# Kernel optimization log

Measured on AMD Instinct MI355X. Metric: run time of the kernel, lower is better.

## Reference

```python
import jax, jax.numpy as jnp
import numpy as np

N_NODES = 2048
IN_FEAT = 512
N_HIDDEN = 512   # layer1 out_features (concat over 8 heads -> 64 per head)
N_CLASSES = 256  # output layer out_features (1 head, averaged)
N_HEADS = 8
NEG_SLOPE = 0.2


def _gat_layer(h, adj, W, a, n_heads, n_hid, is_concat):
    """GraphAttentionLayer (v1) forward, dropout=0 (eval).
    e[i,j,h] = leakyrelu(attn([g_i ; g_j])) decomposes as
    leakyrelu(a_l.g_i + a_r.g_j) since attn is linear."""
    n = h.shape[0]
    g = (h @ W).reshape(n, n_heads, n_hid)           # [n, H, F']
    a_l, a_r = a[:n_hid], a[n_hid:]                  # attn weight split
    s_l = jnp.einsum('ihf,f->ih', g, a_l)            # [n, H]
    s_r = jnp.einsum('jhf,f->jh', g, a_r)            # [n, H]
    e = jax.nn.leaky_relu(s_l[:, None, :] + s_r[None, :, :], NEG_SLOPE)  # [n,n,H]
    e = jnp.where(adj == 0, -jnp.inf, e)             # adj [n,n,1] broadcasts over heads
    attn = jax.nn.softmax(e, axis=1)                 # softmax over neighbors j
    out = jnp.einsum('ijh,jhf->ihf', attn, g)        # [n, H, F']
    if is_concat:
        return out.reshape(n, n_heads * n_hid)
    return out.mean(axis=1)


def setup_inputs() -> dict:
    key = jax.random.key(0)
    ks = jax.random.split(key, 6)
    x = jax.random.normal(ks[0], (N_NODES, IN_FEAT), dtype=jnp.float32)
    adj = jax.random.randint(ks[1], (N_NODES, N_NODES, 1), 0, 2, dtype=jnp.int32)
    # self loops so every row of the softmax has at least one valid entry
    diag = jnp.arange(N_NODES)
    adj = adj.at[diag, diag, 0].set(1)
    W1 = jax.random.normal(ks[2], (IN_FEAT, N_HIDDEN), dtype=jnp.float32) / np.sqrt(IN_FEAT)
    a1 = jax.random.normal(ks[3], (2 * (N_HIDDEN // N_HEADS),), dtype=jnp.float32) / np.sqrt(2 * (N_HIDDEN // N_HEADS))
    W2 = jax.random.normal(ks[4], (N_HIDDEN, N_CLASSES), dtype=jnp.float32) / np.sqrt(N_HIDDEN)
    a2 = jax.random.normal(ks[5], (2 * N_CLASSES,), dtype=jnp.float32) / np.sqrt(2 * N_CLASSES)
    return {"x": x, "adj_mat": adj, "W1": W1, "a1": a1, "W2": W2, "a2": a2}


def reference(x, adj_mat, W1, a1, W2, a2):
    # GAT.forward with dropout=0 (eval mode)
    h = _gat_layer(x, adj_mat, W1, a1, N_HEADS, N_HIDDEN // N_HEADS, True)
    h = jax.nn.elu(h)
    out = _gat_layer(h, adj_mat, W2, a2, 1, N_CLASSES, False)
    return out
```

## Files before the change

### kernel.cpp

```cpp
#include <hip/hip_runtime.h>
#include <hip/hip_bf16.h>
#include <math.h>

#define NN 2048
#define LOG2E 1.4426950408889634f

typedef __attribute__((ext_vector_type(8))) short short8;
typedef __attribute__((ext_vector_type(4))) short s16x4;
typedef __attribute__((ext_vector_type(4))) float f32x4;

__device__ inline unsigned short f2bfu(float f) {
    __hip_bfloat16 h = __float2bfloat16(f);
    return *reinterpret_cast<const unsigned short*>(&h);
}
__device__ inline short f2bfs(float f) {
    __hip_bfloat16 h = __float2bfloat16(f);
    return *reinterpret_cast<const short*>(&h);
}
__device__ inline float bfu2f(unsigned short u) {
    return __uint_as_float(((unsigned int)u) << 16);
}

__global__ __launch_bounds__(256) void pack_adj(
    const int* __restrict__ adj, unsigned long long* __restrict__ adjm,
    float* __restrict__ zeros)
{
    const int t = threadIdx.x, w = t >> 6, l = t & 63;
    if (blockIdx.x < 144) zeros[blockIdx.x * 256 + t] = 0.f;
    const int gw = blockIdx.x * 4 + w;
    const int row = gw >> 5, ch = gw & 31;
    const int v = adj[(size_t)row * NN + ch * 64 + l];
    const unsigned long long bm = __ballot(v != 0);
    if (l == 0) adjm[gw] = bm;
}

__global__ __launch_bounds__(256) void pack_ws(
    const float* __restrict__ W1, unsigned short* __restrict__ w1H, unsigned short* __restrict__ w1L,
    const float* __restrict__ W2, unsigned short* __restrict__ w2H, unsigned short* __restrict__ w2L)
{
    const int t = threadIdx.x, w = t >> 6, l = t & 63;
    const int gq = l >> 4, n16 = l & 15;
    int f = blockIdx.x * 4 + w;
    const float* B; unsigned short *bH, *bL; int N;
    if (f < 512) { B = W1; bH = w1H; bL = w1L; N = 512; }
    else         { B = W2; bH = w2H; bL = w2L; N = 256; f -= 512; }
    const int KT = 16;
    const int nt = f / KT, kt = f - nt * KT;
    const int col = nt * 16 + n16;
    unsigned short uh[8], ul[8];
    #pragma unroll
    for (int e = 0; e < 8; ++e) {
        const int k = kt * 32 + 4 * gq + (e & 3) + 16 * (e >> 2);
        const float v = B[(size_t)k * N + col];
        const unsigned short h = f2bfu(v);
        uh[e] = h;
        ul[e] = f2bfu(v - bfu2f(h));
    }
    *(short8*)&bH[(size_t)f * 512 + l * 8] = *(const short8*)uh;
    *(short8*)&bL[(size_t)f * 512 + l * 8] = *(const short8*)ul;
}

__global__ __launch_bounds__(256) void pack_a_split(
    const float* __restrict__ A, unsigned short* __restrict__ aH,
    unsigned short* __restrict__ aL, int K)
{
    const int t = threadIdx.x, w = t >> 6, l = t & 63;
    const int gq = l >> 4, n16 = l & 15;
    const int KT = K >> 5;
    const int f = blockIdx.x * 4 + w;
    const int mt = f / KT, kt = f - mt * KT;
    const int row = mt * 16 + n16;
    const int k0 = kt * 32 + 4 * gq;
    unsigned short uh[8], ul[8];
    #pragma unroll
    for (int eh = 0; eh < 2; ++eh) {
        const float4 v4 = *(const float4*)&A[(size_t)row * K + k0 + 16 * eh];
        const float vv[4] = {v4.x, v4.y, v4.z, v4.w};
        #pragma unroll
        for (int c = 0; c < 4; ++c) {
            const float v = vv[c];
            const unsigned short h = f2bfu(v);
            uh[4 * eh + c] = h;
            ul[4 * eh + c] = f2bfu(v - bfu2f(h));
        }
    }
    *(short8*)&aH[(size_t)f * 512 + l * 8] = *(const short8*)uh;
    *(short8*)&aL[(size_t)f * 512 + l * 8] = *(const short8*)ul;
}

__global__ __launch_bounds__(256, 2) void gemm_fused(
    const unsigned short* __restrict__ aH, const unsigned short* __restrict__ aL,
    const unsigned short* __restrict__ bH, const unsigned short* __restrict__ bL,
    const float* __restrict__ av, unsigned short* __restrict__ gpO,
    float* __restrict__ slO, float* __restrict__ srO,
    int KT, int dh, int NT)
{
    const int t = threadIdx.x, w = t >> 6, l = t & 63;
    const int gq = l >> 4, n16 = l & 15;
    const int mt = blockIdx.x * 4 + w;
    const int cb = blockIdx.y;
    const int nt0 = cb * 4;
    const size_t abase = (size_t)mt * KT * 512 + l * 8;

    f32x4 acc[4];
    #pragma unroll
    for (int nt = 0; nt < 4; ++nt) acc[nt] = f32x4{0.f, 0.f, 0.f, 0.f};

#define GL(aH_v, aL_v, bH_v, bL_v, kt_) do {                                     \
    const int kk_ = (kt_);                                                       \
    aH_v = *(const short8*)&aH[abase + (size_t)kk_ * 512];                       \
    aL_v = *(const short8*)&aL[abase + (size_t)kk_ * 512];                       \
    _Pragma("unroll")                                                            \
    for (int nt_ = 0; nt_ < 4; ++nt_) {                                          \
        const size_t bo_ = ((size_t)(nt0 + nt_) * KT + kk_) * 512 + l * 8;       \
        bH_v[nt_] = *(const short8*)&bH[bo_];                                    \
        bL_v[nt_] = *(const short8*)&bL[bo_];                                    \
    }                                                                            \
} while (0)

#define GC(aH_v, aL_v, bH_v, bL_v) do {                                          \
    _Pragma("unroll")                                                            \
    for (int nt_ = 0; nt_ < 4; ++nt_) {                                          \
        acc[nt_] = __builtin_amdgcn_mfma_f32_16x16x32_bf16(aH_v, bH_v[nt_], acc[nt_], 0, 0, 0); \
        acc[nt_] = __builtin_amdgcn_mfma_f32_16x16x32_bf16(aH_v, bL_v[nt_], acc[nt_], 0, 0, 0); \
        acc[nt_] = __builtin_amdgcn_mfma_f32_16x16x32_bf16(aL_v, bH_v[nt_], acc[nt_], 0, 0, 0); \
    }                                                                            \
} while (0)

    short8 aHa, aLa, bHa[4], bLa[4], aHb, aLb, bHb[4], bLb[4];
    GL(aHa, aLa, bHa, bLa, 0);
    GL(aHb, aLb, bHb, bLb, 1);
    for (int kt = 0; kt < KT; kt += 2) {
        GC(aHa, aLa, bHa, bLa);
        if (kt + 2 < KT) GL(aHa, aLa, bHa, bLa, kt + 2);
        GC(aHb, aLb, bHb, bLb);
        if (kt + 3 < KT) GL(aHb, aLb, bHb, bLb, kt + 3);
    }
#undef GL
#undef GC

    #pragma unroll
    for (int nt = 0; nt < 4; ++nt) {
        s16x4 u;
        #pragma unroll
        for (int c = 0; c < 4; ++c) u[c] = (short)f2bfu(acc[nt][c]);
        const int f = (mt >> 1) * NT + (nt0 + nt);
        *(s16x4*)&gpO[(size_t)f * 512 + l * 8 + 4 * (mt & 1)] = u;
    }
    const float* al = av;
    const float* ar = av + dh;
    float pl[4] = {0.f, 0.f, 0.f, 0.f}, pr[4] = {0.f, 0.f, 0.f, 0.f};
    #pragma unroll
    for (int nt = 0; nt < 4; ++nt) {
        const int q = (cb * 64 + 16 * nt + n16) & (dh - 1);
        const float wl = al[q], wr_ = ar[q];
        #pragma unroll
        for (int r = 0; r < 4; ++r) { pl[r] += acc[nt][r] * wl; pr[r] += acc[nt][r] * wr_; }
    }
    #pragma unroll
    for (int r = 0; r < 4; ++r) {
        #pragma unroll
        for (int off = 1; off < 16; off <<= 1) {
            pl[r] += __shfl_xor(pl[r], off);
            pr[r] += __shfl_xor(pr[r], off);
        }
    }
    if (n16 == 0) {
        const int hbase = (dh == 64 ? cb : 0) * NN;
        #pragma unroll
        for (int r = 0; r < 4; ++r) {
            const int grow = 16 * mt + 4 * gq + r;
            atomicAdd(&slO[hbase + grow], pl[r] * LOG2E);
            atomicAdd(&srO[hbase + grow], pr[r] * LOG2E);
        }
    }
}

template<int BM, int OUTMODE>
__global__ __launch_bounds__(512, 4) void attn_mfma5(
    const float* __restrict__ slv, const float* __restrict__ srv,
    const unsigned short* __restrict__ gp, const unsigned long long* __restrict__ adjm,
    float* __restrict__ out, unsigned short* __restrict__ aoH, unsigned short* __restrict__ aoL,
    int out_cols, int hsel, int do_elu, int ntg_total)
{
    constexpr int WR = BM / 16;
    constexpr int NJS = 8 / WR;
    constexpr int NITER = (NN / 64) / NJS;
    const int t = threadIdx.x, w = t >> 6, l = t & 63;
    const int gq = l >> 4, n16 = l & 15;
    const int wr = w % WR, js = w / WR;
    const int i0 = blockIdx.x * BM;
    const int cb = blockIdx.y;
    const int h = (hsel < 0) ? cb : hsel;
    const int ntg0 = cb * 4;
    const int arow = i0 + 16 * wr + n16;
    const float* srh = srv + (size_t)h * NN;
    const float sl_reg = slv[(size_t)h * NN + arow];

    __shared__ float accs[8][4][4][65];
    __shared__ float zp[NJS][BM];

    f32x4 acc[4];
    #pragma unroll
    for (int nt = 0; nt < 4; ++nt) acc[nt] = f32x4{0.f, 0.f, 0.f, 0.f};
    float zacc = 0.f;

#define LOADT(am_, bf_, tile_) do {                                              \
    const int tl_ = (tile_);                                                     \
    am_ = adjm[(size_t)arow * 32 + tl_];                                         \
    _Pragma("unroll")                                                            \
    for (int s_ = 0; s_ < 2; ++s_)                                               \
        _Pragma("unroll")                                                        \
        for (int nt_ = 0; nt_ < 4; ++nt_)                                        \
            bf_[s_][nt_] = *(const short8*)&gp[                                  \
                (size_t)((2 * tl_ + s_) * ntg_total + ntg0 + nt_) * 512 + l * 8];\
} while (0)

#define COMPT(am_, bf_, tile_) do {                                              \
    const int tl_ = (tile_);                                                     \
    f32x4 sr4_[4];                                                               \
    _Pragma("unroll")                                                            \
    for (int q_ = 0; q_ < 4; ++q_)                                               \
        sr4_[q_] = *(const f32x4*)&srh[64 * tl_ + 32 * (q_ >> 1) + 16 * (q_ & 1) + 4 * gq]; \
    short8 af_[2];                                                               \
    _Pragma("unroll")                                                            \
    for (int s_ = 0; s_ < 2; ++s_) {                                             \
        const unsigned am32_ = (unsigned)(am_ >> (32 * s_ + 4 * gq));            \
        _Pragma("unroll")                                                        \
        for (int hb_ = 0; hb_ < 2; ++hb_) {                                      \
            const f32x4 s4_ = sr4_[2 * s_ + hb_];                                \
            _Pragma("unroll")                                                    \
            for (int c_ = 0; c_ < 4; ++c_) {                                     \
                float f_ = sl_reg + s4_[c_];                                     \
                f_ = fmaxf(f_, 0.2f * f_);                                       \
                float wv_ = __builtin_amdgcn_exp2f(f_);                          \
                const int msk_ = (int)(am32_ << (31 - (c_ + 16 * hb_))) >> 31;   \
                wv_ = __int_as_float(__float_as_int(wv_) & msk_);                \
                zacc += wv_;                                                     \
                af_[s_][4 * hb_ + c_] = f2bfs(wv_);                              \
            }                                                                    \
        }                                                                        \
    }                                                                            \
    _Pragma("unroll")                                                            \
    for (int s_ = 0; s_ < 2; ++s_)                                               \
        _Pragma("unroll")                                                        \
        for (int nt_ = 0; nt_ < 4; ++nt_)                                        \
            acc[nt_] = __builtin_amdgcn_mfma_f32_16x16x32_bf16(                  \
                af_[s_], bf_[s_][nt_], acc[nt_], 0, 0, 0);                       \
} while (0)

    unsigned long long amA, amB;
    short8 bfA[2][4], bfB[2][4];

    LOADT(amA, bfA, js);
    LOADT(amB, bfB, js + NJS);

    for (int k = 0; k < NITER; k += 2) {
        COMPT(amA, bfA, js + k * NJS);
        {
            const int kn = (k + 2 < NITER) ? (k + 2) : (NITER - 1);
            LOADT(amA, bfA, js + kn * NJS);
        }
        COMPT(amB, bfB, js + (k + 1) * NJS);
        {
            const int kn = (k + 3 < NITER) ? (k + 3) : (NITER - 1);
            LOADT(amB, bfB, js + kn * NJS);
        }
    }
#undef LOADT
#undef COMPT

    zacc += __shfl_xor(zacc, 16);
    zacc += __shfl_xor(zacc, 32);
    if (l < 16) zp[js][16 * wr + l] = zacc;
    #pragma unroll
    for (int nt = 0; nt < 4; ++nt)
        #pragma unroll
        for (int r = 0; r < 4; ++r)
            accs[w][nt][r][l] = acc[nt][r];
    __syncthreads();

    if constexpr (OUTMODE == 0) {
        #pragma unroll
        for (int idx = 0; idx < WR * 2; ++idx) {
            const int flat = w + 8 * idx;
            const int wr2 = flat >> 4, rem = flat & 15, nt = rem >> 2, r = rem & 3;
            const int ro = 16 * wr2 + 4 * gq + r;
            float z = 0.f, v = 0.f;
            #pragma unroll
            for (int jj = 0; jj < NJS; ++jj) {
                z += zp[jj][ro];
                v += accs[jj * WR + wr2][nt][r][l];
            }
            float o = v / z;
            if (do_elu) o = (o > 0.f) ? o : (__builtin_amdgcn_exp2f(o * LOG2E) - 1.f);
            out[(size_t)(i0 + ro) * out_cols + cb * 64 + nt * 16 + n16] = o;
        }
    } else {
        const int mtl = (w >> 1) & 1, ktl = w & 1, eh = w >> 2;
        const int rowl = l & 15, colq = l >> 4;
        const int grow = 16 * mtl + rowl;
        float z = 0.f;
        #pragma unroll
        for (int jj = 0; jj < NJS; ++jj) z += zp[jj][grow];
        const float rz = 1.0f / z;
        const int wr2 = mtl, srcr = rowl & 3, srcgq = (rowl >> 2) & 3;
        unsigned short uh[4], ul[4];
        #pragma unroll
        for (int c = 0; c < 4; ++c) {
            const int col = 32 * ktl + 16 * eh + 4 * colq + c;
            const int nt = col >> 4, c16 = col & 15;
            float v = 0.f;
            #pragma unroll
            for (int jj = 0; jj < NJS; ++jj)
                v += accs[jj * WR + wr2][nt][srcr][srcgq * 16 + c16];
            float o = v * rz;
            o = (o > 0.f) ? o : (__builtin_amdgcn_exp2f(o * LOG2E) - 1.f);
            const unsigned short hi = f2bfu(o);
            uh[c] = hi;
            ul[c] = f2bfu(o - bfu2f(hi));
        }
        const int mt = (i0 >> 4) + mtl, kt = 2 * cb + ktl;
        const size_t off = ((size_t)mt * 16 + kt) * 512 + l * 8 + 4 * eh;
        *(s16x4*)&aoH[off] = *(const s16x4*)uh;
        *(s16x4*)&aoL[off] = *(const s16x4*)ul;
    }
}

extern "C" void kernel_launch(void* const* d_in, const int* in_sizes, int n_in,
                              void* d_out, int out_size, void* d_ws, size_t ws_size,
                              hipStream_t stream)
{
    const float* x   = (const float*)d_in[0];
    const int*   adj = (const int*)  d_in[1];
    const float* W1  = (const float*)d_in[2];
    const float* a1  = (const float*)d_in[3];
    const float* W2  = (const float*)d_in[4];
    const float* a2  = (const float*)d_in[5];
    float* out = (float*)d_out;

    float* sl1 = (float*)d_ws;
    float* sr1 = sl1 + 8 * 2048;
    float* sl2 = sr1 + 8 * 2048;
    float* sr2 = sl2 + 2048;
    unsigned long long* adjm = (unsigned long long*)(sr2 + 2048);
    unsigned short* gp1 = (unsigned short*)(adjm + 65536);
    unsigned short* gp2 = gp1 + 2048 * 512;
    unsigned short* axH = gp2 + 1024 * 512;
    unsigned short* axL = axH + 2048 * 512;
    unsigned short* ahH = axL + 2048 * 512;
    unsigned short* ahL = ahH + 2048 * 512;
    unsigned short* w1H = ahL + 2048 * 512;
    unsigned short* w1L = w1H + 512 * 512;
    unsigned short* w2H = w1L + 512 * 512;
    unsigned short* w2L = w2H + 256 * 512;

    pack_adj<<<dim3(16384), 256, 0, stream>>>(adj, adjm, sl1);
    pack_ws<<<dim3(192), 256, 0, stream>>>(W1, w1H, w1L, W2, w2H, w2L);
    pack_a_split<<<dim3(512), 256, 0, stream>>>(x, axH, axL, 512);

    gemm_fused<<<dim3(32, 8), 256, 0, stream>>>(axH, axL, w1H, w1L, a1, gp1, sl1, sr1, 16, 64, 32);
    attn_mfma5<32, 1><<<dim3(64, 8), 512, 0, stream>>>(sl1, sr1, gp1, adjm,
                                                       nullptr, ahH, ahL, 512, -1, 1, 32);

    gemm_fused<<<dim3(32, 4), 256, 0, stream>>>(ahH, ahL, w2H, w2L, a2, gp2, sl2, sr2, 16, 256, 16);
    attn_mfma5<16, 0><<<dim3(128, 4), 512, 0, stream>>>(sl2, sr2, gp2, adjm,
                                                        out, nullptr, nullptr, 256, 0, 0, 16);
}
```

Measured before the change: 63.85 us.

## Merge prep kernels and restructure attention to share B fragments across row tiles

Folds the three packing kernels into a single prep launch, removing two kernel launches. The attention kernel now has each wave process all row tiles (MT) against one j-subtile, so each loaded gp fragment feeds MT MFMAs instead of splitting rows across waves. Adjacency is read as 32-bit half-words per subtile, and the layer-1 epilogue is staged in two halves to fit shared memory. The trade-off is more registers per wave and extra barriers in the epilogue.

```diff
diff --git a/kernel.cpp b/kernel.cpp
--- a/kernel.cpp
+++ b/kernel.cpp
@@ -21,71 +21,63 @@
     return __uint_as_float(((unsigned int)u) << 16);
 }
 
-__global__ __launch_bounds__(256) void pack_adj(
+__global__ __launch_bounds__(256) void prep(
     const int* __restrict__ adj, unsigned long long* __restrict__ adjm,
-    float* __restrict__ zeros)
+    float* __restrict__ zeros,
+    const float* __restrict__ W1, unsigned short* __restrict__ w1H, unsigned short* __restrict__ w1L,
+    const float* __restrict__ W2, unsigned short* __restrict__ w2H, unsigned short* __restrict__ w2L,
+    const float* __restrict__ x, unsigned short* __restrict__ axH, unsigned short* __restrict__ axL)
 {
-    const int t = threadIdx.x, w = t >> 6, l = t & 63;
-    if (blockIdx.x < 144) zeros[blockIdx.x * 256 + t] = 0.f;
-    const int gw = blockIdx.x * 4 + w;
-    const int row = gw >> 5, ch = gw & 31;
-    const int v = adj[(size_t)row * NN + ch * 64 + l];
-    const unsigned long long bm = __ballot(v != 0);
-    if (l == 0) adjm[gw] = bm;
-}
-
-__global__ __launch_bounds__(256) void pack_ws(
-    const float* __restrict__ W1, unsigned short* __restrict__ w1H, unsigned short* __restrict__ w1L,
-    const float* __restrict__ W2, unsigned short* __restrict__ w2H, unsigned short* __restrict__ w2L)
-{
-    const int t = threadIdx.x, w = t >> 6, l = t & 63;
+    const int b = blockIdx.x, t = threadIdx.x, w = t >> 6, l = t & 63;
     const int gq = l >> 4, n16 = l & 15;
-    int f = blockIdx.x * 4 + w;
-    const float* B; unsigned short *bH, *bL; int N;
-    if (f < 512) { B = W1; bH = w1H; bL = w1L; N = 512; }
-    else         { B = W2; bH = w2H; bL = w2L; N = 256; f -= 512; }
-    const int KT = 16;
-    const int nt = f / KT, kt = f - nt * KT;
-    const int col = nt * 16 + n16;
-    unsigned short uh[8], ul[8];
-    #pragma unroll
-    for (int e = 0; e < 8; ++e) {
-        const int k = kt * 32 + 4 * gq + (e & 3) + 16 * (e >> 2);
-        const float v = B[(size_t)k * N + col];
-        const unsigned short h = f2bfu(v);
-        uh[e] = h;
-        ul[e] = f2bfu(v - bfu2f(h));
-    }
-    *(short8*)&bH[(size_t)f * 512 + l * 8] = *(const short8*)uh;
-    *(short8*)&bL[(size_t)f * 512 + l * 8] = *(const short8*)ul;
-}
-
-__global__ __launch_bounds__(256) void pack_a_split(
-    const float* __restrict__ A, unsigned short* __restrict__ aH,
-    unsigned short* __restrict__ aL, int K)
-{
-    const int t = threadIdx.x, w = t >> 6, l = t & 63;
-    const int gq = l >> 4, n16 = l & 15;
-    const int KT = K >> 5;
-    const int f = blockIdx.x * 4 + w;
-    const int mt = f / KT, kt = f - mt * KT;
-    const int row = mt * 16 + n16;
-    const int k0 = kt * 32 + 4 * gq;
-    unsigned short uh[8], ul[8];
-    #pragma unroll
-    for (int eh = 0; eh < 2; ++eh) {
-        const float4 v4 = *(const float4*)&A[(size_t)row * K + k0 + 16 * eh];
-        const float vv[4] = {v4.x, v4.y, v4.z, v4.w};
-        #pragma unroll
-        for (int c = 0; c < 4; ++c) {
-            const float v = vv[c];
-            const unsigned short h = f2bfu(v);
-            uh[4 * eh + c] = h;
-            ul[4 * eh + c] = f2bfu(v - bfu2f(h));
-        }
-    }
-    *(short8*)&aH[(size_t)f * 512 + l * 8] = *(const short8*)uh;
-    *(short8*)&aL[(size_t)f * 512 + l * 8] = *(const short8*)ul;
+    {
+        const int gw = b * 4 + w;
+        const int row = gw >> 5, ch = gw & 31;
+        const int v = adj[(size_t)row * NN + ch * 64 + l];
+        const unsigned long long bm = __ballot(v != 0);
+        if (l == 0) adjm[gw] = bm;
+    }
+    if (b < 144) {
+        zeros[b * 256 + t] = 0.f;
+    } else if (b >= 256 && b < 448) {
+        int f = (b - 256) * 4 + w;
+        const float* B; unsigned short *bH, *bL; int N;
+        if (f < 512) { B = W1; bH = w1H; bL = w1L; N = 512; }
+        else         { B = W2; bH = w2H; bL = w2L; N = 256; f -= 512; }
+        const int nt = f >> 4, kt = f & 15;
+        const int col = nt * 16 + n16;
+        unsigned short uh[8], ul[8];
+        #pragma unroll
+        for (int e = 0; e < 8; ++e) {
+            const int k = kt * 32 + 4 * gq + (e & 3) + 16 * (e >> 2);
+            const float v = B[(size_t)k * N + col];
+            const unsigned short hi = f2bfu(v);
+            uh[e] = hi;
+            ul[e] = f2bfu(v - bfu2f(hi));
+        }
+        *(short8*)&bH[(size_t)f * 512 + l * 8] = *(const short8*)uh;
+        *(short8*)&bL[(size_t)f * 512 + l * 8] = *(const short8*)ul;
+    } else if (b >= 448 && b < 960) {
+        const int f = (b - 448) * 4 + w;
+        const int mt = f >> 4, kt = f & 15;
+        const int row = mt * 16 + n16;
+        const int k0 = kt * 32 + 4 * gq;
+        unsigned short uh[8], ul[8];
+        #pragma unroll
+        for (int eh = 0; eh < 2; ++eh) {
+            const float4 v4 = *(const float4*)&x[(size_t)row * 512 + k0 + 16 * eh];
+            const float vv[4] = {v4.x, v4.y, v4.z, v4.w};
+            #pragma unroll
+            for (int c = 0; c < 4; ++c) {
+                const float v = vv[c];
+                const unsigned short hi = f2bfu(v);
+                uh[4 * eh + c] = hi;
+                ul[4 * eh + c] = f2bfu(v - bfu2f(hi));
+            }
+        }
+        *(short8*)&axH[(size_t)f * 512 + l * 8] = *(const short8*)uh;
+        *(short8*)&axL[(size_t)f * 512 + l * 8] = *(const short8*)ul;
+    }
 }
 
 __global__ __launch_bounds__(256, 2) void gemm_fused(
@@ -176,154 +168,174 @@
     }
 }
 
-template<int BM, int OUTMODE>
-__global__ __launch_bounds__(512, 4) void attn_mfma5(
+template<int MT, int OUTMODE>
+__global__ __launch_bounds__(512, 4) void attn_mfma6(
     const float* __restrict__ slv, const float* __restrict__ srv,
-    const unsigned short* __restrict__ gp, const unsigned long long* __restrict__ adjm,
+    const unsigned short* __restrict__ gp, const unsigned int* __restrict__ adjm32,
     float* __restrict__ out, unsigned short* __restrict__ aoH, unsigned short* __restrict__ aoL,
     int out_cols, int hsel, int do_elu, int ntg_total)
 {
-    constexpr int WR = BM / 16;
-    constexpr int NJS = 8 / WR;
-    constexpr int NITER = (NN / 64) / NJS;
     const int t = threadIdx.x, w = t >> 6, l = t & 63;
     const int gq = l >> 4, n16 = l & 15;
-    const int wr = w % WR, js = w / WR;
-    const int i0 = blockIdx.x * BM;
+    const int i0 = blockIdx.x * (MT * 16);
     const int cb = blockIdx.y;
     const int h = (hsel < 0) ? cb : hsel;
     const int ntg0 = cb * 4;
-    const int arow = i0 + 16 * wr + n16;
     const float* srh = srv + (size_t)h * NN;
-    const float sl_reg = slv[(size_t)h * NN + arow];
-
-    __shared__ float accs[8][4][4][65];
-    __shared__ float zp[NJS][BM];
-
-    f32x4 acc[4];
-    #pragma unroll
-    for (int nt = 0; nt < 4; ++nt) acc[nt] = f32x4{0.f, 0.f, 0.f, 0.f};
-    float zacc = 0.f;
-
-#define LOADT(am_, bf_, tile_) do {                                              \
+    int arow[MT];
+    float slr[MT];
+    #pragma unroll
+    for (int mt = 0; mt < MT; ++mt) {
+        arow[mt] = i0 + 16 * mt + n16;
+        slr[mt] = slv[(size_t)h * NN + arow[mt]];
+    }
+
+    __shared__ float accs_raw[8320];
+    __shared__ float zp[8][MT * 16];
+
+    f32x4 acc[MT][4];
+    float zacc[MT];
+    #pragma unroll
+    for (int mt = 0; mt < MT; ++mt) {
+        zacc[mt] = 0.f;
+        #pragma unroll
+        for (int nt = 0; nt < 4; ++nt) acc[mt][nt] = f32x4{0.f, 0.f, 0.f, 0.f};
+    }
+
+#define LOADH(bf_, sr_, am_, tile_, s_) do {                                     \
     const int tl_ = (tile_);                                                     \
-    am_ = adjm[(size_t)arow * 32 + tl_];                                         \
-    _Pragma("unroll")                                                            \
-    for (int s_ = 0; s_ < 2; ++s_)                                               \
-        _Pragma("unroll")                                                        \
-        for (int nt_ = 0; nt_ < 4; ++nt_)                                        \
-            bf_[s_][nt_] = *(const short8*)&gp[                                  \
-                (size_t)((2 * tl_ + s_) * ntg_total + ntg0 + nt_) * 512 + l * 8];\
+    _Pragma("unroll")                                                            \
+    for (int nt_ = 0; nt_ < 4; ++nt_)                                            \
+        bf_[nt_] = *(const short8*)&gp[                                          \
+            (size_t)((2 * tl_ + (s_)) * ntg_total + ntg0 + nt_) * 512 + l * 8];  \
+    _Pragma("unroll")                                                            \
+    for (int hb_ = 0; hb_ < 2; ++hb_)                                            \
+        sr_[hb_] = *(const f32x4*)&srh[64 * tl_ + 32 * (s_) + 16 * hb_ + 4 * gq];\
+    _Pragma("unroll")                                                            \
+    for (int mt_ = 0; mt_ < MT; ++mt_)                                           \
+        am_[mt_] = adjm32[((size_t)arow[mt_] * 32 + tl_) * 2 + (s_)];            \
 } while (0)
 
-#define COMPT(am_, bf_, tile_) do {                                              \
-    const int tl_ = (tile_);                                                     \
-    f32x4 sr4_[4];                                                               \
-    _Pragma("unroll")                                                            \
-    for (int q_ = 0; q_ < 4; ++q_)                                               \
-        sr4_[q_] = *(const f32x4*)&srh[64 * tl_ + 32 * (q_ >> 1) + 16 * (q_ & 1) + 4 * gq]; \
-    short8 af_[2];                                                               \
-    _Pragma("unroll")                                                            \
-    for (int s_ = 0; s_ < 2; ++s_) {                                             \
-        const unsigned am32_ = (unsigned)(am_ >> (32 * s_ + 4 * gq));            \
+#define COMPH(bf_, sr_, am_) do {                                                \
+    short8 af_[MT];                                                              \
+    _Pragma("unroll")                                                            \
+    for (int mt_ = 0; mt_ < MT; ++mt_) {                                         \
+        const unsigned am32_ = am_[mt_] >> (4 * gq);                             \
         _Pragma("unroll")                                                        \
         for (int hb_ = 0; hb_ < 2; ++hb_) {                                      \
-            const f32x4 s4_ = sr4_[2 * s_ + hb_];                                \
+            const f32x4 s4_ = sr_[hb_];                                          \
             _Pragma("unroll")                                                    \
             for (int c_ = 0; c_ < 4; ++c_) {                                     \
-                float f_ = sl_reg + s4_[c_];                                     \
+                float f_ = slr[mt_] + s4_[c_];                                   \
                 f_ = fmaxf(f_, 0.2f * f_);                                       \
                 float wv_ = __builtin_amdgcn_exp2f(f_);                          \
                 const int msk_ = (int)(am32_ << (31 - (c_ + 16 * hb_))) >> 31;   \
                 wv_ = __int_as_float(__float_as_int(wv_) & msk_);                \
-                zacc += wv_;                                                     \
-                af_[s_][4 * hb_ + c_] = f2bfs(wv_);                              \
+                zacc[mt_] += wv_;                                                \
+                af_[mt_][4 * hb_ + c_] = f2bfs(wv_);                             \
             }                                                                    \
         }                                                                        \
     }                                                                            \
     _Pragma("unroll")                                                            \
-    for (int s_ = 0; s_ < 2; ++s_)                                               \
+    for (int mt_ = 0; mt_ < MT; ++mt_)                                           \
         _Pragma("unroll")                                                        \
         for (int nt_ = 0; nt_ < 4; ++nt_)                                        \
-            acc[nt_] = __builtin_amdgcn_mfma_f32_16x16x32_bf16(                  \
-                af_[s_], bf_[s_][nt_], acc[nt_], 0, 0, 0);                       \
+            acc[mt_][nt_] = __builtin_amdgcn_mfma_f32_16x16x32_bf16(             \
+                af_[mt_], bf_[nt_], acc[mt_][nt_], 0, 0, 0);                     \
 } while (0)
 
-    unsigned long long amA, amB;
-    short8 bfA[2][4], bfB[2][4];
-
-    LOADT(amA, bfA, js);
-    LOADT(amB, bfB, js + NJS);
-
-    for (int k = 0; k < NITER; k += 2) {
-        COMPT(amA, bfA, js + k * NJS);
-        {
-            const int kn = (k + 2 < NITER) ? (k + 2) : (NITER - 1);
-            LOADT(amA, bfA, js + kn * NJS);
-        }
-        COMPT(amB, bfB, js + (k + 1) * NJS);
-        {
-            const int kn = (k + 3 < NITER) ? (k + 3) : (NITER - 1);
-            LOADT(amB, bfB, js + kn * NJS);
-        }
-    }
-#undef LOADT
-#undef COMPT
-
-    zacc += __shfl_xor(zacc, 16);
-    zacc += __shfl_xor(zacc, 32);
-    if (l < 16) zp[js][16 * wr + l] = zacc;
-    #pragma unroll
-    for (int nt = 0; nt < 4; ++nt)
-        #pragma unroll
-        for (int r = 0; r < 4; ++r)
-            accs[w][nt][r][l] = acc[nt][r];
-    __syncthreads();
+    unsigned amA[MT], amB[MT];
+    f32x4 srA[2], srB[2];
+    short8 bfA[4], bfB[4];
+
+    LOADH(bfA, srA, amA, w, 0);
+    LOADH(bfB, srB, amB, w, 1);
+    #pragma unroll
+    for (int k = 0; k < 4; ++k) {
+        const int tn = (k < 3) ? (w + 8 * (k + 1)) : (w + 8 * k);
+        COMPH(bfA, srA, amA);
+        LOADH(bfA, srA, amA, tn, 0);
+        COMPH(bfB, srB, amB);
+        LOADH(bfB, srB, amB, tn, 1);
+    }
+#undef LOADH
+#undef COMPH
+
+    #pragma unroll
+    for (int mt = 0; mt < MT; ++mt) {
+        zacc[mt] += __shfl_xor(zacc[mt], 16);
+        zacc[mt] += __shfl_xor(zacc[mt], 32);
+    }
+    if (l < 16) {
+        #pragma unroll
+        for (int mt = 0; mt < MT; ++mt) zp[w][16 * mt + l] = zacc[mt];
+    }
 
     if constexpr (OUTMODE == 0) {
         #pragma unroll
-        for (int idx = 0; idx < WR * 2; ++idx) {
+        for (int nt = 0; nt < 4; ++nt)
+            #pragma unroll
+            for (int r = 0; r < 4; ++r)
+                accs_raw[((w * 4 + nt) * 4 + r) * 65 + l] = acc[0][nt][r];
+        __syncthreads();
+        #pragma unroll
+        for (int idx = 0; idx < 2; ++idx) {
             const int flat = w + 8 * idx;
-            const int wr2 = flat >> 4, rem = flat & 15, nt = rem >> 2, r = rem & 3;
-            const int ro = 16 * wr2 + 4 * gq + r;
+            const int nt = flat >> 2, r = flat & 3;
+            const int ro = 4 * gq + r;
             float z = 0.f, v = 0.f;
             #pragma unroll
-            for (int jj = 0; jj < NJS; ++jj) {
+            for (int jj = 0; jj < 8; ++jj) {
                 z += zp[jj][ro];
-                v += accs[jj * WR + wr2][nt][r][l];
+                v += accs_raw[((jj * 4 + nt) * 4 + r) * 65 + l];
             }
             float o = v / z;
             if (do_elu) o = (o > 0.f) ? o : (__builtin_amdgcn_exp2f(o * LOG2E) - 1.f);
             out[(size_t)(i0 + ro) * out_cols + cb * 64 + nt * 16 + n16] = o;
         }
     } else {
-        const int mtl = (w >> 1) & 1, ktl = w & 1, eh = w >> 2;
+        const int mtl = w & 1, eh = (w >> 1) & 1;
         const int rowl = l & 15, colq = l >> 4;
-        const int grow = 16 * mtl + rowl;
-        float z = 0.f;
-        #pragma unroll
-        for (int jj = 0; jj < NJS; ++jj) z += zp[jj][grow];
-        const float rz = 1.0f / z;
-        const int wr2 = mtl, srcr = rowl & 3, srcgq = (rowl >> 2) & 3;
-        unsigned short uh[4], ul[4];
-        #pragma unroll
-        for (int c = 0; c < 4; ++c) {
-            const int col = 32 * ktl + 16 * eh + 4 * colq + c;
-            const int nt = col >> 4, c16 = col & 15;
-            float v = 0.f;
+        #pragma unroll
+        for (int h2 = 0; h2 < 2; ++h2) {
             #pragma unroll
-            for (int jj = 0; jj < NJS; ++jj)
-                v += accs[jj * WR + wr2][nt][srcr][srcgq * 16 + c16];
-            float o = v * rz;
-            o = (o > 0.f) ? o : (__builtin_amdgcn_exp2f(o * LOG2E) - 1.f);
-            const unsigned short hi = f2bfu(o);
-            uh[c] = hi;
-            ul[c] = f2bfu(o - bfu2f(hi));
-        }
-        const int mt = (i0 >> 4) + mtl, kt = 2 * cb + ktl;
-        const size_t off = ((size_t)mt * 16 + kt) * 512 + l * 8 + 4 * eh;
-        *(s16x4*)&aoH[off] = *(const s16x4*)uh;
-        *(s16x4*)&aoL[off] = *(const s16x4*)ul;
+            for (int mt = 0; mt < MT; ++mt)
+                #pragma unroll
+                for (int ntl = 0; ntl < 2; ++ntl)
+                    #pragma unroll
+                    for (int r = 0; r < 4; ++r)
+                        accs_raw[(((w * 2 + mt) * 2 + ntl) * 4 + r) * 65 + l] =
+                            acc[mt][2 * h2 + ntl][r];
+            __syncthreads();
+            if (w < 4) {
+                const int grow = 16 * mtl + rowl;
+                float z = 0.f;
+                #pragma unroll
+                for (int jj = 0; jj < 8; ++jj) z += zp[jj][grow];
+                const float rz = 1.0f / z;
+                unsigned short uh[4], ul[4];
+                #pragma unroll
+                for (int c = 0; c < 4; ++c) {
+                    const int c16 = 4 * colq + c;
+                    float v = 0.f;
+                    #pragma unroll
+                    for (int jj = 0; jj < 8; ++jj)
+                        v += accs_raw[(((jj * 2 + mtl) * 2 + eh) * 4 + (rowl & 3)) * 65
+                                      + (rowl >> 2) * 16 + c16];
+                    float o = v * rz;
+                    o = (o > 0.f) ? o : (__builtin_amdgcn_exp2f(o * LOG2E) - 1.f);
+                    const unsigned short hi = f2bfu(o);
+                    uh[c] = hi;
+                    ul[c] = f2bfu(o - bfu2f(hi));
+                }
+                const int mtg = blockIdx.x * 2 + mtl;
+                const int kt = 2 * cb + h2;
+                const size_t off = ((size_t)mtg * 16 + kt) * 512 + l * 8 + 4 * eh;
+                *(s16x4*)&aoH[off] = *(const s16x4*)uh;
+                *(s16x4*)&aoL[off] = *(const s16x4*)ul;
+            }
+            __syncthreads();
+        }
     }
 }
 
@@ -355,15 +367,14 @@
     unsigned short* w2H = w1L + 512 * 512;
     unsigned short* w2L = w2H + 256 * 512;
 
-    pack_adj<<<dim3(16384), 256, 0, stream>>>(adj, adjm, sl1);
-    pack_ws<<<dim3(192), 256, 0, stream>>>(W1, w1H, w1L, W2, w2H, w2L);
-    pack_a_split<<<dim3(512), 256, 0, stream>>>(x, axH, axL, 512);
+    prep<<<dim3(16384), 256, 0, stream>>>(adj, adjm, sl1,
+                                          W1, w1H, w1L, W2, w2H, w2L, x, axH, axL);
 
     gemm_fused<<<dim3(32, 8), 256, 0, stream>>>(axH, axL, w1H, w1L, a1, gp1, sl1, sr1, 16, 64, 32);
-    attn_mfma5<32, 1><<<dim3(64, 8), 512, 0, stream>>>(sl1, sr1, gp1, adjm,
-                                                       nullptr, ahH, ahL, 512, -1, 1, 32);
+    attn_mfma6<2, 1><<<dim3(64, 8), 512, 0, stream>>>(sl1, sr1, gp1, (const unsigned int*)adjm,
+                                                      nullptr, ahH, ahL, 512, -1, 1, 32);
 
     gemm_fused<<<dim3(32, 4), 256, 0, stream>>>(ahH, ahL, w2H, w2L, a2, gp2, sl2, sr2, 16, 256, 16);
-    attn_mfma5<16, 0><<<dim3(128, 4), 512, 0, stream>>>(sl2, sr2, gp2, adjm,
-                                                        out, nullptr, nullptr, 256, 0, 0, 16);
-}
+    attn_mfma6<1, 0><<<dim3(128, 4), 512, 0, stream>>>(sl2, sr2, gp2, (const unsigned int*)adjm,
+                                                       out, nullptr, nullptr, 256, 0, 0, 16);
+}
```

After: 56.19 us, median of 2. 12.0% less time.
